# Performance work log

Hardware: AMD Instinct MI355X
Metric: run time of the kernel (lower is better)

Reference implementation:

```python
import jax, jax.numpy as jnp
import numpy as np

N_NODES = 100000
N_EDGES = 640000
IN_FEATS = 256
HEADS = 4
OUT_FEATS = 32
NEG_SLOPE = 0.2


def setup_inputs() -> dict:
    key = jax.random.key(0)
    k_feat, k_src, k_dst, k_w, k_al, k_ar = jax.random.split(key, 6)
    feat = jax.random.normal(k_feat, (N_NODES, IN_FEATS), dtype=jnp.float32)
    src = jax.random.randint(k_src, (N_EDGES,), 0, N_NODES, dtype=jnp.int32)
    dst = jax.random.randint(k_dst, (N_EDGES,), 0, N_NODES, dtype=jnp.int32)
    # fc: Linear(in_feats, out_feats*num_heads, bias=False); store as [in, H*D]
    W = jax.random.normal(k_w, (IN_FEATS, HEADS * OUT_FEATS), dtype=jnp.float32) * 0.05
    attn_l = jax.random.normal(k_al, (HEADS, OUT_FEATS), dtype=jnp.float32) * 0.1
    attn_r = jax.random.normal(k_ar, (HEADS, OUT_FEATS), dtype=jnp.float32) * 0.1
    return {"feat": feat, "W": W, "attn_l": attn_l, "attn_r": attn_r, "src": src, "dst": dst}


def reference(feat, W, attn_l, attn_r, src, dst):
    N = feat.shape[0]
    H, D = attn_l.shape
    # fc + reshape to [N, H, D]
    ft = (feat @ W).reshape(N, H, D)
    # per-node attention logits [N, H]
    el = jnp.einsum('nhd,hd->nh', ft, attn_l)
    er = jnp.einsum('nhd,hd->nh', ft, attn_r)
    # u_add_v then leaky relu -> per-edge logits [E, H]
    e = el[src] + er[dst]
    e = jnp.where(e > 0, e, NEG_SLOPE * e)
    # edge softmax over incoming edges of each dst node (per head)
    m = jax.ops.segment_max(e, dst, num_segments=N)  # [N, H]
    m = jnp.where(jnp.isfinite(m), m, jnp.zeros_like(m))  # empty segments
    ex = jnp.exp(e - m[dst])
    denom = jax.ops.segment_sum(ex, dst, num_segments=N)  # [N, H]
    a = ex / denom[dst]  # [E, H]
    # u_mul_e + sum aggregation: rst[v] = sum_{(u,v)} a_uv * ft[u]
    msg = ft[src] * a[:, :, None]  # [E, H, D]
    rst = jax.ops.segment_sum(msg, dst, num_segments=N)  # [N, H, D]
    return rst, a[:, :, None]
```

## Files before the change

kernel.cpp:

```cpp
#include <hip/hip_runtime.h>

#define N_NODES 100000
#define N_EDGES 640000
#define IN_F 256
#define HD 128

using f32x4 = __attribute__((ext_vector_type(4))) float;
using s8v   = __attribute__((ext_vector_type(8))) short;

__device__ __forceinline__ unsigned short bf16rn(float x) {
  unsigned u = __builtin_bit_cast(unsigned, x);
  return (unsigned short)((u + 0x7FFFu + ((u >> 16) & 1u)) >> 16);
}
__device__ __forceinline__ float bf16tof(unsigned short h) {
  unsigned u = ((unsigned)h) << 16;
  return __builtin_bit_cast(float, u);
}

__global__ __launch_bounds__(256) void prep_b(const float* __restrict__ W,
    short* __restrict__ Bth, short* __restrict__ Btl)
{
  int t = threadIdx.x;
  int c = t >> 1;
  int kbase = (t & 1) * 128;
  #pragma unroll 8
  for (int kk = 0; kk < 128; ++kk) {
    int k = kbase + kk;
    float w = W[(size_t)k * HD + c];
    unsigned short h = bf16rn(w);
    unsigned short l = bf16rn(w - bf16tof(h));
    Bth[(size_t)c * IN_F + k] = (short)h;
    Btl[(size_t)c * IN_F + k] = (short)l;
  }
}

__global__ __launch_bounds__(256) void gemm_mfma(const float* __restrict__ feat,
    const short* __restrict__ Bth, const short* __restrict__ Btl,
    float* __restrict__ ft, int M)
{
  const int wid  = threadIdx.x >> 6;
  const int lane = threadIdx.x & 63;
  const int lr = lane & 15;
  const int lg = lane >> 4;
  const int wm = (wid >> 1) * 64;
  const int wn = (wid & 1) * 64;
  const int rb = blockIdx.x * 128;

  f32x4 acc[4][4];
  #pragma unroll
  for (int i = 0; i < 4; i++)
    #pragma unroll
    for (int j = 0; j < 4; j++) acc[i][j] = (f32x4){0.f, 0.f, 0.f, 0.f};

  int rowg[4];
  #pragma unroll
  for (int mi = 0; mi < 4; mi++) {
    int r = rb + wm + mi * 16 + lr;
    rowg[mi] = r < M ? r : M - 1;
  }

  #pragma unroll
  for (int kt = 0; kt < 8; ++kt) {
    const int k0 = kt * 32;
    s8v bh[4], bl[4];
    #pragma unroll
    for (int ni = 0; ni < 4; ni++) {
      int c = wn + ni * 16 + lr;
      bh[ni] = *(const s8v*)(Bth + (size_t)c * IN_F + k0 + lg * 8);
      bl[ni] = *(const s8v*)(Btl + (size_t)c * IN_F + k0 + lg * 8);
    }
    #pragma unroll
    for (int mi = 0; mi < 4; mi++) {
      const float* ap = feat + (size_t)rowg[mi] * IN_F + k0 + lg * 8;
      const float4 a0 = *(const float4*)ap;
      const float4 a1 = *(const float4*)(ap + 4);
      float av[8] = {a0.x, a0.y, a0.z, a0.w, a1.x, a1.y, a1.z, a1.w};
      s8v ah, al;
      #pragma unroll
      for (int j = 0; j < 8; j++) {
        unsigned short h = bf16rn(av[j]);
        ah[j] = (short)h;
        al[j] = (short)bf16rn(av[j] - bf16tof(h));
      }
      #pragma unroll
      for (int ni = 0; ni < 4; ni++) {
        acc[mi][ni] = __builtin_amdgcn_mfma_f32_16x16x32_bf16(ah, bh[ni], acc[mi][ni], 0, 0, 0);
        acc[mi][ni] = __builtin_amdgcn_mfma_f32_16x16x32_bf16(ah, bl[ni], acc[mi][ni], 0, 0, 0);
        acc[mi][ni] = __builtin_amdgcn_mfma_f32_16x16x32_bf16(al, bh[ni], acc[mi][ni], 0, 0, 0);
      }
    }
  }

  #pragma unroll
  for (int mi = 0; mi < 4; mi++) {
    int rbase = rb + wm + mi * 16 + lg * 4;
    #pragma unroll
    for (int ni = 0; ni < 4; ni++) {
      int col = wn + ni * 16 + lr;
      #pragma unroll
      for (int r = 0; r < 4; r++) {
        int grow = rbase + r;
        if (grow < M) ft[(size_t)grow * HD + col] = acc[mi][ni][r];
      }
    }
  }
}

__global__ __launch_bounds__(256) void elr_kernel(const float* __restrict__ ft,
    const float* __restrict__ al, const float* __restrict__ ar,
    float* __restrict__ el, float* __restrict__ er, int n)
{
  int v = blockIdx.x * 4 + (threadIdx.x >> 6);
  if (v >= n) return;
  int lane = threadIdx.x & 63;
  float f0 = ft[(size_t)v * HD + lane], f1 = ft[(size_t)v * HD + 64 + lane];
  float l0 = f0 * al[lane],      l1 = f1 * al[64 + lane];
  float r0 = f0 * ar[lane],      r1 = f1 * ar[64 + lane];
  #pragma unroll
  for (int off = 16; off >= 1; off >>= 1) {
    l0 += __shfl_xor(l0, off); l1 += __shfl_xor(l1, off);
    r0 += __shfl_xor(r0, off); r1 += __shfl_xor(r1, off);
  }
  if ((lane & 31) == 0) {
    int g = lane >> 5;
    el[v * 4 + g] = l0; el[v * 4 + 2 + g] = l1;
    er[v * 4 + g] = r0; er[v * 4 + 2 + g] = r1;
  }
}

__global__ void deg_kernel(const int* __restrict__ dst, int* __restrict__ deg) {
  int i = blockIdx.x * blockDim.x + threadIdx.x;
  if (i < N_EDGES) atomicAdd(&deg[dst[i]], 1);
}

__global__ __launch_bounds__(256) void scanA(const int* __restrict__ deg,
    int* __restrict__ excl, int* __restrict__ partials, int n)
{
  __shared__ int s[256];
  int t = threadIdx.x;
  int base = blockIdx.x * 1024 + t * 4;
  int d0 = (base + 0 < n) ? deg[base + 0] : 0;
  int d1 = (base + 1 < n) ? deg[base + 1] : 0;
  int d2 = (base + 2 < n) ? deg[base + 2] : 0;
  int d3 = (base + 3 < n) ? deg[base + 3] : 0;
  int sum = d0 + d1 + d2 + d3;
  s[t] = sum; __syncthreads();
  for (int off = 1; off < 256; off <<= 1) {
    int x = 0; if (t >= off) x = s[t - off];
    __syncthreads(); s[t] += x; __syncthreads();
  }
  int e0 = s[t] - sum;
  if (base + 0 < n) excl[base + 0] = e0;
  if (base + 1 < n) excl[base + 1] = e0 + d0;
  if (base + 2 < n) excl[base + 2] = e0 + d0 + d1;
  if (base + 3 < n) excl[base + 3] = e0 + d0 + d1 + d2;
  if (t == 255) partials[blockIdx.x] = s[255];
}

__global__ void scanB(int* partials, int nb) {
  __shared__ int s[128];
  int t = threadIdx.x;
  int v = (t < nb) ? partials[t] : 0;
  s[t] = v; __syncthreads();
  for (int off = 1; off < 128; off <<= 1) {
    int x = 0; if (t >= off) x = s[t - off];
    __syncthreads(); s[t] += x; __syncthreads();
  }
  if (t < nb) partials[t] = s[t] - v;
}

__global__ __launch_bounds__(256) void scanC(int* __restrict__ row_ptr,
    const int* __restrict__ partials, int n, int E)
{
  int t = threadIdx.x;
  int base = blockIdx.x * 1024 + t * 4;
  int add = partials[blockIdx.x];
  #pragma unroll
  for (int j = 0; j < 4; j++) if (base + j < n) row_ptr[base + j] += add;
  if (blockIdx.x == 0 && t == 0) row_ptr[n] = E;
}

__global__ void scatter_kernel(const int* __restrict__ src, const int* __restrict__ dst,
                               const int* __restrict__ row_ptr,
                               int* __restrict__ cursor, int* __restrict__ usrc) {
  int e = blockIdx.x * blockDim.x + threadIdx.x;
  if (e >= N_EDGES) return;
  int d = dst[e];
  int pos = row_ptr[d] + atomicAdd(&cursor[d], 1);
  usrc[pos] = src[e];
}

__global__ __launch_bounds__(256) void gat_node(const int* __restrict__ row_ptr,
    const int* __restrict__ usrc,
    const float* __restrict__ el, const float* __restrict__ er4,
    const float* __restrict__ ft, float* __restrict__ rst,
    float* __restrict__ lse, int n)
{
  __shared__ int   su[4][64];
  __shared__ float sex[4][64][4];
  const int w = threadIdx.x >> 6;
  const int lane = threadIdx.x & 63;
  const int v = blockIdx.x * 4 + w;
  if (v >= n) return;
  const int s0 = row_ptr[v];
  const int d  = row_ptr[v + 1] - s0;
  const int g  = lane >> 4;

  if (d == 0) {
    *(float2*)(rst + (size_t)v * HD + 2 * lane) = make_float2(0.f, 0.f);
    return;
  }

  const float4 erv = *(const float4*)(er4 + (size_t)v * 4);
  float m0 = -1e30f, m1 = -1e30f, m2 = -1e30f, m3 = -1e30f;
  float den = 0.f;
  float2 acc = make_float2(0.f, 0.f);

  for (int c0 = 0; c0 < d; c0 += 64) {
    const int cd = min(64, d - c0);
    float x0 = -1e30f, x1 = -1e30f, x2 = -1e30f, x3 = -1e30f;
    int u = 0;
    if (lane < cd) {
      u = usrc[s0 + c0 + lane];
      const float4 elv = *(const float4*)(el + (size_t)u * 4);
      x0 = elv.x + erv.x; x0 = x0 > 0.f ? x0 : 0.2f * x0;
      x1 = elv.y + erv.y; x1 = x1 > 0.f ? x1 : 0.2f * x1;
      x2 = elv.z + erv.z; x2 = x2 > 0.f ? x2 : 0.2f * x2;
      x3 = elv.w + erv.w; x3 = x3 > 0.f ? x3 : 0.2f * x3;
    }
    su[w][lane] = u;
    float n0 = x0, n1 = x1, n2 = x2, n3 = x3;
    #pragma unroll
    for (int off = 32; off >= 1; off >>= 1) {
      n0 = fmaxf(n0, __shfl_xor(n0, off));
      n1 = fmaxf(n1, __shfl_xor(n1, off));
      n2 = fmaxf(n2, __shfl_xor(n2, off));
      n3 = fmaxf(n3, __shfl_xor(n3, off));
    }
    n0 = fmaxf(n0, m0); n1 = fmaxf(n1, m1); n2 = fmaxf(n2, m2); n3 = fmaxf(n3, m3);
    float e0 = __expf(x0 - n0), e1 = __expf(x1 - n1);
    float e2 = __expf(x2 - n2), e3 = __expf(x3 - n3);
    sex[w][lane][0] = e0; sex[w][lane][1] = e1;
    sex[w][lane][2] = e2; sex[w][lane][3] = e3;
    float mg = g == 0 ? m0 : g == 1 ? m1 : g == 2 ? m2 : m3;
    float ng = g == 0 ? n0 : g == 1 ? n1 : g == 2 ? n2 : n3;
    float scale = __expf(mg - ng);
    den *= scale; acc.x *= scale; acc.y *= scale;
    m0 = n0; m1 = n1; m2 = n2; m3 = n3;
    asm volatile("s_waitcnt lgkmcnt(0)" ::: "memory");
    #pragma unroll 4
    for (int j = 0; j < cd; ++j) {
      int uu = su[w][j];
      float wgt = sex[w][j][g];
      float2 f = *(const float2*)(ft + (size_t)uu * HD + 2 * lane);
      den += wgt;
      acc.x += wgt * f.x; acc.y += wgt * f.y;
    }
  }
  *(float2*)(rst + (size_t)v * HD + 2 * lane) = make_float2(acc.x / den, acc.y / den);
  if ((lane & 15) == 0) {
    float mg = g == 0 ? m0 : g == 1 ? m1 : g == 2 ? m2 : m3;
    lse[(size_t)v * 4 + g] = mg + __logf(den);
  }
}

__global__ void norm_kernel(const int* __restrict__ src, const int* __restrict__ dst,
                            const float* __restrict__ el, const float* __restrict__ er,
                            const float* __restrict__ lse, float* __restrict__ a, int E)
{
  int i = blockIdx.x * blockDim.x + threadIdx.x;
  if (i >= E) return;
  int u = src[i], v = dst[i];
  const float4 elv = *(const float4*)(el + (size_t)u * 4);
  const float4 erv = *(const float4*)(er + (size_t)v * 4);
  const float4 ls  = *(const float4*)(lse + (size_t)v * 4);
  float x0 = elv.x + erv.x; x0 = x0 > 0.f ? x0 : 0.2f * x0;
  float x1 = elv.y + erv.y; x1 = x1 > 0.f ? x1 : 0.2f * x1;
  float x2 = elv.z + erv.z; x2 = x2 > 0.f ? x2 : 0.2f * x2;
  float x3 = elv.w + erv.w; x3 = x3 > 0.f ? x3 : 0.2f * x3;
  float4 o;
  o.x = __expf(x0 - ls.x); o.y = __expf(x1 - ls.y);
  o.z = __expf(x2 - ls.z); o.w = __expf(x3 - ls.w);
  *(float4*)(a + (size_t)i * 4) = o;
}

extern "C" void kernel_launch(void* const* d_in, const int* in_sizes, int n_in,
                              void* d_out, int out_size, void* d_ws, size_t ws_size,
                              hipStream_t stream)
{
  const float* feat = (const float*)d_in[0];
  const float* W    = (const float*)d_in[1];
  const float* al   = (const float*)d_in[2];
  const float* ar   = (const float*)d_in[3];
  const int*   src  = (const int*)d_in[4];
  const int*   dst  = (const int*)d_in[5];
  float* rst   = (float*)d_out;
  float* a_out = rst + (size_t)N_NODES * HD;

  char* w = (char*)d_ws;
  auto alloc = [&](size_t bytes) { char* p = w; w += (bytes + 255) & ~(size_t)255; return p; };
  float* ft      = (float*)alloc((size_t)N_NODES * HD * 4);
  float* el      = (float*)alloc((size_t)N_NODES * 4 * 4);
  float* er      = (float*)alloc((size_t)N_NODES * 4 * 4);
  float* lse     = (float*)alloc((size_t)N_NODES * 4 * 4);
  int*   deg     = (int*)alloc((size_t)N_NODES * 4);
  int*   row_ptr = (int*)alloc(((size_t)N_NODES + 1) * 4);
  int*   cursor  = (int*)alloc((size_t)N_NODES * 4);
  int*   partials= (int*)alloc(1024);
  int*   usrc    = (int*)alloc((size_t)N_EDGES * 4);
  short* Bth     = (short*)alloc((size_t)HD * IN_F * 2);
  short* Btl     = (short*)alloc((size_t)HD * IN_F * 2);

  hipMemsetAsync(deg, 0, N_NODES * 4, stream);
  hipMemsetAsync(cursor, 0, N_NODES * 4, stream);

  prep_b<<<1, 256, 0, stream>>>(W, Bth, Btl);
  gemm_mfma<<<(N_NODES + 127) / 128, 256, 0, stream>>>(feat, Bth, Btl, ft, N_NODES);
  elr_kernel<<<(N_NODES + 3) / 4, 256, 0, stream>>>(ft, al, ar, el, er, N_NODES);
  deg_kernel<<<(N_EDGES + 255) / 256, 256, 0, stream>>>(dst, deg);
  scanA<<<98, 256, 0, stream>>>(deg, row_ptr, partials, N_NODES);
  scanB<<<1, 128, 0, stream>>>(partials, 98);
  scanC<<<98, 256, 0, stream>>>(row_ptr, partials, N_NODES, N_EDGES);
  scatter_kernel<<<(N_EDGES + 255) / 256, 256, 0, stream>>>(src, dst, row_ptr, cursor, usrc);
  gat_node<<<(N_NODES + 3) / 4, 256, 0, stream>>>(row_ptr, usrc, el, er, ft, rst, lse, N_NODES);
  norm_kernel<<<(N_EDGES + 255) / 256, 256, 0, stream>>>(src, dst, el, er, lse, a_out, N_EDGES);
}
```

Measured before the change: 427.6 us.

## Fuse attention logit projection into GEMM and drop low-order weight split

Folds attn_l/attn_r into W so el/er are produced by extra MFMAs inside the feature GEMM, removing the separate elr kernel and its re-read of ft. The weight's low bf16 half is dropped (3 MFMAs per tile become 2), the GEMM tile shrinks to 64 rows for more blocks, and A/B loads are software-prefetched across k steps. Accuracy drops slightly because W is now only bf16, and el/er are computed from the folded weights rather than the rounded ft.

```diff
diff --git a/kernel.cpp b/kernel.cpp
--- a/kernel.cpp
+++ b/kernel.cpp
@@ -1,4 +1,5 @@
 #include <hip/hip_runtime.h>
+#include <hip/hip_bf16.h>
 
 #define N_NODES 100000
 #define N_EDGES 640000
@@ -8,91 +9,128 @@
 using f32x4 = __attribute__((ext_vector_type(4))) float;
 using s8v   = __attribute__((ext_vector_type(8))) short;
 
-__device__ __forceinline__ unsigned short bf16rn(float x) {
-  unsigned u = __builtin_bit_cast(unsigned, x);
-  return (unsigned short)((u + 0x7FFFu + ((u >> 16) & 1u)) >> 16);
-}
-__device__ __forceinline__ float bf16tof(unsigned short h) {
-  unsigned u = ((unsigned)h) << 16;
+__device__ __forceinline__ short bf16h(float x) {
+  __hip_bfloat16 h = __float2bfloat16(x);
+  return (short)__builtin_bit_cast(unsigned short, h);
+}
+__device__ __forceinline__ float bf16tof(short h) {
+  unsigned u = ((unsigned)(unsigned short)h) << 16;
   return __builtin_bit_cast(float, u);
 }
 
 __global__ __launch_bounds__(256) void prep_b(const float* __restrict__ W,
-    short* __restrict__ Bth, short* __restrict__ Btl)
-{
-  int t = threadIdx.x;
-  int c = t >> 1;
-  int kbase = (t & 1) * 128;
-  #pragma unroll 8
-  for (int kk = 0; kk < 128; ++kk) {
-    int k = kbase + kk;
-    float w = W[(size_t)k * HD + c];
-    unsigned short h = bf16rn(w);
-    unsigned short l = bf16rn(w - bf16tof(h));
-    Bth[(size_t)c * IN_F + k] = (short)h;
-    Btl[(size_t)c * IN_F + k] = (short)l;
-  }
+                                              short* __restrict__ Bth)
+{
+  int c = blockIdx.x;
+  int k = threadIdx.x;
+  Bth[(size_t)c * IN_F + k] = bf16h(W[(size_t)k * HD + c]);
+}
+
+__global__ __launch_bounds__(256) void prep_x(const float* __restrict__ W,
+    const float* __restrict__ al, const float* __restrict__ ar,
+    short* __restrict__ Bxh)
+{
+  int c = blockIdx.x;
+  int k = threadIdx.x;
+  float v = 0.f;
+  if (c < 8) {
+    int h = c & 3;
+    const float* att = (c < 4) ? al : ar;
+    #pragma unroll
+    for (int d = 0; d < 32; d++)
+      v += W[(size_t)k * HD + h * 32 + d] * att[h * 32 + d];
+  }
+  Bxh[(size_t)c * IN_F + k] = bf16h(v);
 }
 
 __global__ __launch_bounds__(256) void gemm_mfma(const float* __restrict__ feat,
-    const short* __restrict__ Bth, const short* __restrict__ Btl,
-    float* __restrict__ ft, int M)
+    const short* __restrict__ Bth, const short* __restrict__ Bxh,
+    float* __restrict__ ft, float* __restrict__ el, float* __restrict__ er, int M)
 {
   const int wid  = threadIdx.x >> 6;
   const int lane = threadIdx.x & 63;
   const int lr = lane & 15;
   const int lg = lane >> 4;
-  const int wm = (wid >> 1) * 64;
+  const int wm = (wid >> 1) * 32;
   const int wn = (wid & 1) * 64;
-  const int rb = blockIdx.x * 128;
-
-  f32x4 acc[4][4];
-  #pragma unroll
-  for (int i = 0; i < 4; i++)
-    #pragma unroll
-    for (int j = 0; j < 4; j++) acc[i][j] = (f32x4){0.f, 0.f, 0.f, 0.f};
-
-  int rowg[4];
-  #pragma unroll
-  for (int mi = 0; mi < 4; mi++) {
+  const int rb = blockIdx.x * 64;
+  const bool doX = (wid & 1) == 0;
+
+  f32x4 acc[2][4];
+  f32x4 accx[2];
+  #pragma unroll
+  for (int mi = 0; mi < 2; mi++) {
+    accx[mi] = (f32x4){0.f, 0.f, 0.f, 0.f};
+    #pragma unroll
+    for (int ni = 0; ni < 4; ni++) acc[mi][ni] = (f32x4){0.f, 0.f, 0.f, 0.f};
+  }
+
+  const float* ap[2];
+  #pragma unroll
+  for (int mi = 0; mi < 2; mi++) {
     int r = rb + wm + mi * 16 + lr;
-    rowg[mi] = r < M ? r : M - 1;
-  }
+    if (r > M - 1) r = M - 1;
+    ap[mi] = feat + (size_t)r * IN_F + lg * 8;
+  }
+  const short* bp[4];
+  #pragma unroll
+  for (int ni = 0; ni < 4; ni++)
+    bp[ni] = Bth + (size_t)(wn + ni * 16 + lr) * IN_F + lg * 8;
+  const short* xp = Bxh + (size_t)lr * IN_F + lg * 8;
+
+  float4 A0[3][2], A1[3][2];
+  s8v Bb[2][4], Xb[2];
+
+  #pragma unroll
+  for (int mi = 0; mi < 2; mi++) {
+    A0[0][mi] = *(const float4*)(ap[mi]);       A1[0][mi] = *(const float4*)(ap[mi] + 4);
+    A0[1][mi] = *(const float4*)(ap[mi] + 32);  A1[1][mi] = *(const float4*)(ap[mi] + 36);
+  }
+  #pragma unroll
+  for (int ni = 0; ni < 4; ni++) Bb[0][ni] = *(const s8v*)(bp[ni]);
+  Xb[0] = *(const s8v*)xp;
 
   #pragma unroll
   for (int kt = 0; kt < 8; ++kt) {
-    const int k0 = kt * 32;
-    s8v bh[4], bl[4];
-    #pragma unroll
-    for (int ni = 0; ni < 4; ni++) {
-      int c = wn + ni * 16 + lr;
-      bh[ni] = *(const s8v*)(Bth + (size_t)c * IN_F + k0 + lg * 8);
-      bl[ni] = *(const s8v*)(Btl + (size_t)c * IN_F + k0 + lg * 8);
-    }
-    #pragma unroll
-    for (int mi = 0; mi < 4; mi++) {
-      const float* ap = feat + (size_t)rowg[mi] * IN_F + k0 + lg * 8;
-      const float4 a0 = *(const float4*)ap;
-      const float4 a1 = *(const float4*)(ap + 4);
-      float av[8] = {a0.x, a0.y, a0.z, a0.w, a1.x, a1.y, a1.z, a1.w};
-      s8v ah, al;
+    const int cur = kt % 3, pre = (kt + 2) % 3;
+    const int curb = kt & 1, preb = curb ^ 1;
+    if (kt + 2 < 8) {
+      #pragma unroll
+      for (int mi = 0; mi < 2; mi++) {
+        A0[pre][mi] = *(const float4*)(ap[mi] + (kt + 2) * 32);
+        A1[pre][mi] = *(const float4*)(ap[mi] + (kt + 2) * 32 + 4);
+      }
+    }
+    if (kt + 1 < 8) {
+      #pragma unroll
+      for (int ni = 0; ni < 4; ni++) Bb[preb][ni] = *(const s8v*)(bp[ni] + (kt + 1) * 32);
+      Xb[preb] = *(const s8v*)(xp + (kt + 1) * 32);
+    }
+    #pragma unroll
+    for (int mi = 0; mi < 2; mi++) {
+      const float av[8] = {A0[cur][mi].x, A0[cur][mi].y, A0[cur][mi].z, A0[cur][mi].w,
+                           A1[cur][mi].x, A1[cur][mi].y, A1[cur][mi].z, A1[cur][mi].w};
+      s8v ah, alo;
       #pragma unroll
       for (int j = 0; j < 8; j++) {
-        unsigned short h = bf16rn(av[j]);
-        ah[j] = (short)h;
-        al[j] = (short)bf16rn(av[j] - bf16tof(h));
+        short h = bf16h(av[j]);
+        ah[j]  = h;
+        alo[j] = bf16h(av[j] - bf16tof(h));
       }
       #pragma unroll
       for (int ni = 0; ni < 4; ni++) {
-        acc[mi][ni] = __builtin_amdgcn_mfma_f32_16x16x32_bf16(ah, bh[ni], acc[mi][ni], 0, 0, 0);
-        acc[mi][ni] = __builtin_amdgcn_mfma_f32_16x16x32_bf16(ah, bl[ni], acc[mi][ni], 0, 0, 0);
-        acc[mi][ni] = __builtin_amdgcn_mfma_f32_16x16x32_bf16(al, bh[ni], acc[mi][ni], 0, 0, 0);
-      }
-    }
-  }
-
-  #pragma unroll
-  for (int mi = 0; mi < 4; mi++) {
+        acc[mi][ni] = __builtin_amdgcn_mfma_f32_16x16x32_bf16(ah,  Bb[curb][ni], acc[mi][ni], 0, 0, 0);
+        acc[mi][ni] = __builtin_amdgcn_mfma_f32_16x16x32_bf16(alo, Bb[curb][ni], acc[mi][ni], 0, 0, 0);
+      }
+      if (doX) {
+        accx[mi] = __builtin_amdgcn_mfma_f32_16x16x32_bf16(ah,  Xb[curb], accx[mi], 0, 0, 0);
+        accx[mi] = __builtin_amdgcn_mfma_f32_16x16x32_bf16(alo, Xb[curb], accx[mi], 0, 0, 0);
+      }
+    }
+  }
+
+  #pragma unroll
+  for (int mi = 0; mi < 2; mi++) {
     int rbase = rb + wm + mi * 16 + lg * 4;
     #pragma unroll
     for (int ni = 0; ni < 4; ni++) {
@@ -103,28 +141,16 @@
         if (grow < M) ft[(size_t)grow * HD + col] = acc[mi][ni][r];
       }
     }
-  }
-}
-
-__global__ __launch_bounds__(256) void elr_kernel(const float* __restrict__ ft,
-    const float* __restrict__ al, const float* __restrict__ ar,
-    float* __restrict__ el, float* __restrict__ er, int n)
-{
-  int v = blockIdx.x * 4 + (threadIdx.x >> 6);
-  if (v >= n) return;
-  int lane = threadIdx.x & 63;
-  float f0 = ft[(size_t)v * HD + lane], f1 = ft[(size_t)v * HD + 64 + lane];
-  float l0 = f0 * al[lane],      l1 = f1 * al[64 + lane];
-  float r0 = f0 * ar[lane],      r1 = f1 * ar[64 + lane];
-  #pragma unroll
-  for (int off = 16; off >= 1; off >>= 1) {
-    l0 += __shfl_xor(l0, off); l1 += __shfl_xor(l1, off);
-    r0 += __shfl_xor(r0, off); r1 += __shfl_xor(r1, off);
-  }
-  if ((lane & 31) == 0) {
-    int g = lane >> 5;
-    el[v * 4 + g] = l0; el[v * 4 + 2 + g] = l1;
-    er[v * 4 + g] = r0; er[v * 4 + 2 + g] = r1;
+    if (doX) {
+      #pragma unroll
+      for (int r = 0; r < 4; r++) {
+        int grow = rbase + r;
+        if (grow < M) {
+          if (lr < 4)      el[(size_t)grow * 4 + lr]       = accx[mi][r];
+          else if (lr < 8) er[(size_t)grow * 4 + (lr - 4)] = accx[mi][r];
+        }
+      }
+    }
   }
 }
 
@@ -309,14 +335,14 @@
   int*   partials= (int*)alloc(1024);
   int*   usrc    = (int*)alloc((size_t)N_EDGES * 4);
   short* Bth     = (short*)alloc((size_t)HD * IN_F * 2);
-  short* Btl     = (short*)alloc((size_t)HD * IN_F * 2);
+  short* Bxh     = (short*)alloc((size_t)16 * IN_F * 2);
 
   hipMemsetAsync(deg, 0, N_NODES * 4, stream);
   hipMemsetAsync(cursor, 0, N_NODES * 4, stream);
 
-  prep_b<<<1, 256, 0, stream>>>(W, Bth, Btl);
-  gemm_mfma<<<(N_NODES + 127) / 128, 256, 0, stream>>>(feat, Bth, Btl, ft, N_NODES);
-  elr_kernel<<<(N_NODES + 3) / 4, 256, 0, stream>>>(ft, al, ar, el, er, N_NODES);
+  prep_b<<<128, 256, 0, stream>>>(W, Bth);
+  prep_x<<<16, 256, 0, stream>>>(W, al, ar, Bxh);
+  gemm_mfma<<<(N_NODES + 63) / 64, 256, 0, stream>>>(feat, Bth, Bxh, ft, el, er, N_NODES);
   deg_kernel<<<(N_EDGES + 255) / 256, 256, 0, stream>>>(dst, deg);
   scanA<<<98, 256, 0, stream>>>(deg, row_ptr, partials, N_NODES);
   scanB<<<1, 128, 0, stream>>>(partials, 98);
```

After: 364.4 us. -14.8%, faster.
